# Kernel optimization log

Measured on AMD Instinct MI355X. Metric: run time of the kernel, lower is better.

## Reference

```python
import jax, jax.numpy as jnp
import numpy as np

EPS = 1e-6


def setup_inputs() -> dict:
    key = jax.random.key(0)
    k_x, k_qkv, k_proj = jax.random.split(key, 3)
    B, C, H, W, D = 4, 256, 16, 16, 16
    x = jax.random.normal(k_x, (B, C, H, W, D), dtype=jnp.float32)
    # 1x1 Conv3d == per-position linear; init roughly like torch conv default
    fan_in = C
    bound = 1.0 / np.sqrt(fan_in)
    qkv_w = jax.random.uniform(k_qkv, (3 * C, C), jnp.float32, -bound, bound)
    qkv_b = jnp.zeros((3 * C,), jnp.float32)
    proj_w = jax.random.uniform(k_proj, (C, C), jnp.float32, -bound, bound)
    proj_b = jnp.zeros((C,), jnp.float32)
    norm_gamma = jnp.ones((C,), jnp.float32)
    norm_beta = jnp.zeros((C,), jnp.float32)
    return {"x": x, "norm_gamma": norm_gamma, "norm_beta": norm_beta,
            "qkv_w": qkv_w, "qkv_b": qkv_b, "proj_w": proj_w, "proj_b": proj_b}


def reference(x, norm_gamma, norm_beta, qkv_w, qkv_b, proj_w, proj_b):
    B, C, H, W, D = x.shape
    N = H * W * D
    scale = float(C) ** -0.5

    # GroupNorm with num_groups=1: normalize over (C,H,W,D) per sample (biased var)
    mean = jnp.mean(x, axis=(1, 2, 3, 4), keepdims=True)
    var = jnp.mean(jnp.square(x - mean), axis=(1, 2, 3, 4), keepdims=True)
    xn = (x - mean) * jax.lax.rsqrt(var + EPS)
    xn = xn * norm_gamma[None, :, None, None, None] + norm_beta[None, :, None, None, None]

    xn_flat = xn.reshape(B, C, N)  # b c n
    # 1x1 conv == channel-mixing GEMM
    qkv = jnp.einsum('oc,bcn->bon', qkv_w, xn_flat) + qkv_b[None, :, None]  # [B, 3C, N]
    q, k, v = jnp.split(qkv, 3, axis=1)  # each [B, C, N]

    w = jnp.einsum('bcq,bck->bqk', q, k) * scale  # [B, N, N]
    w = jax.nn.softmax(w, axis=-1)
    h = jnp.einsum('bqk,bck->bcq', w, v)  # [B, C, N]

    h = jnp.einsum('oc,bcn->bon', proj_w, h) + proj_b[None, :, None]
    return x + h.reshape(B, C, H, W, D)
```

## Files before the change

### kernel.cpp

```cpp
#include <hip/hip_runtime.h>

typedef __attribute__((ext_vector_type(8))) short short8;
typedef __attribute__((ext_vector_type(4))) float f32x4;
typedef __attribute__((ext_vector_type(16))) float f32x16;
typedef __attribute__((ext_vector_type(4))) int i32x4;

__device__ __forceinline__ unsigned short f2bf(float f){
  union { float f; unsigned int u; } cv; cv.f = f;
  unsigned int u = cv.u;
  u = (u + 0x7fffu + ((u >> 16) & 1u)) >> 16;
  return (unsigned short)u;
}
__device__ __forceinline__ float bf2f(unsigned short h){
  union { unsigned int u; float f; } cv; cv.u = ((unsigned int)h) << 16;
  return cv.f;
}

typedef unsigned int u32g __attribute__((address_space(1)));
typedef unsigned int u32l __attribute__((address_space(3)));
__device__ __forceinline__ void gload16(const void* g, void* l){
  __builtin_amdgcn_global_load_lds((const u32g*)g, (u32l*)l, 16, 0, 0);
}

__device__ __forceinline__ unsigned int cvtpk_bf16(float lo, float hi){
  unsigned int r;
  asm("v_cvt_pk_bf16_f32 %0, %1, %2" : "=v"(r) : "v"(lo), "v"(hi));
  return r;
}
__device__ __forceinline__ unsigned int cvt2_fp8(float a, float b){
  unsigned int r;
  asm("v_cvt_pk_fp8_f32 %0, %1, %2" : "=v"(r) : "v"(a), "v"(b));
  return r;
}

#define BARRIER() asm volatile("s_barrier" ::: "memory")
#define WAITV(N)  asm volatile("s_waitcnt vmcnt(" #N ")" ::: "memory")
#define WAITLGKM0() asm volatile("s_waitcnt lgkmcnt(0)" ::: "memory")

__global__ __launch_bounds__(256) void fused_pre_k(const float* __restrict__ x,
                                                   float2* __restrict__ partial,
                                                   const float* __restrict__ qkv_w,
                                                   const float* __restrict__ qkv_b,
                                                   const float* __restrict__ proj_w,
                                                   unsigned short* __restrict__ Wqk,
                                                   unsigned short* __restrict__ Wv,
                                                   unsigned short* __restrict__ Wp,
                                                   float* __restrict__ bias_qk){
  const int blk = blockIdx.x;
  if (blk < 256){
    const int b = blk >> 6, xb = blk & 63;
    const float4* xp = (const float4*)(x + (size_t)b*1048576 + (size_t)xb*16384);
    float s = 0.f, sq = 0.f;
    #pragma unroll
    for (int i = 0; i < 16; ++i){
      float4 v = xp[threadIdx.x + i*256];
      s  += v.x + v.y + v.z + v.w;
      sq += v.x*v.x + v.y*v.y + v.z*v.z + v.w*v.w;
    }
    #pragma unroll
    for (int m = 1; m < 64; m <<= 1){ s += __shfl_xor(s, m); sq += __shfl_xor(sq, m); }
    __shared__ float2 acc[4];
    if ((threadIdx.x & 63) == 0) acc[threadIdx.x >> 6] = make_float2(s, sq);
    __syncthreads();
    if (threadIdx.x == 0){
      float S = 0.f, Q = 0.f;
      for (int i = 0; i < 4; ++i){ S += acc[i].x; Q += acc[i].y; }
      partial[b*64 + xb] = make_float2(S, Q);
    }
  } else {
    int id = (blk - 256) * 256 + threadIdx.x;
    if (id < 131072){
      Wqk[id] = f2bf(qkv_w[id]);
      if (id < 512) bias_qk[id] = qkv_b[id];
    } else if (id < 196608){
      Wv[id - 131072] = f2bf(qkv_w[id]);
    } else {
      int j = id - 196608;
      Wp[j] = f2bf(proj_w[j]);
    }
  }
}

__global__ __launch_bounds__(256) void norm_transpose_k(const float* __restrict__ x,
                                                        const float* __restrict__ gamma,
                                                        const float* __restrict__ beta,
                                                        const float2* __restrict__ partial,
                                                        unsigned short* __restrict__ xnt){
  __shared__ float tile[64][65];
  __shared__ float2 stt;
  const int b = blockIdx.z, n0 = blockIdx.x*64, c0 = blockIdx.y*64;
  const int t = threadIdx.x;
  if (t < 64){
    float2 p = partial[b*64 + t];
    float s = p.x, q = p.y;
    #pragma unroll
    for (int m = 1; m < 64; m <<= 1){ s += __shfl_xor(s, m); q += __shfl_xor(q, m); }
    if (t == 0){
      const float inv = 1.0f/1048576.0f;
      float mean = s*inv;
      float var  = q*inv - mean*mean;
      stt = make_float2(mean, rsqrtf(var + 1e-6f));
    }
  }
  __syncthreads();
  const float2 st = stt;
  const int col = t & 63, rb = t >> 6;
  #pragma unroll
  for (int i = 0; i < 16; ++i){
    int rr = i*4 + rb;
    float xv = x[((size_t)b*256 + c0 + rr)*4096 + n0 + col];
    tile[rr][col] = (xv - st.x) * st.y * gamma[c0+rr] + beta[c0+rr];
  }
  __syncthreads();
  #pragma unroll
  for (int i = 0; i < 16; ++i){
    int nr = i*4 + rb;
    xnt[((size_t)b*4096 + n0 + nr)*256 + c0 + col] = f2bf(tile[col][nr]);
  }
}

__global__ __launch_bounds__(256) void gemm_nt_k(const unsigned short* __restrict__ A,
                                                 const unsigned short* __restrict__ B,
                                                 int lda, int ldb, long sA, long sB,
                                                 const float* __restrict__ bias_m,
                                                 const float* __restrict__ bias_n,
                                                 const float* __restrict__ resid, long sR,
                                                 float* __restrict__ outF,
                                                 unsigned short* __restrict__ outB,
                                                 unsigned char* __restrict__ out8,
                                                 int ldc, long sC, int vtile){
  __shared__ unsigned short As[64][40];
  __shared__ unsigned short Bs[64][40];
  const int b  = blockIdx.z;
  const int m0 = blockIdx.x * 64, n0 = blockIdx.y * 64;
  const unsigned short* Ab = A + (size_t)b * sA;
  const unsigned short* Bb = B + (size_t)b * sB;
  const int t = threadIdx.x;
  const int lane = t & 63, w = t >> 6;
  const int g = lane >> 4, r = lane & 15;
  const int wm = (w >> 1) * 32, wn = (w & 1) * 32;
  const int lrow = t >> 2, lcol = (t & 3) * 8;
  f32x4 acc00 = {0,0,0,0}, acc01 = {0,0,0,0}, acc10 = {0,0,0,0}, acc11 = {0,0,0,0};
  for (int ks = 0; ks < 8; ++ks){
    short8 av = *(const short8*)(Ab + (size_t)(m0 + lrow) * lda + ks*32 + lcol);
    short8 bv = *(const short8*)(Bb + (size_t)(n0 + lrow) * ldb + ks*32 + lcol);
    __syncthreads();
    *(short8*)&As[lrow][lcol] = av;
    *(short8*)&Bs[lrow][lcol] = bv;
    __syncthreads();
    short8 af0 = *(const short8*)&As[wm + r][g*8];
    short8 af1 = *(const short8*)&As[wm + 16 + r][g*8];
    short8 bf0 = *(const short8*)&Bs[wn + r][g*8];
    short8 bf1 = *(const short8*)&Bs[wn + 16 + r][g*8];
    acc00 = __builtin_amdgcn_mfma_f32_16x16x32_bf16(af0, bf0, acc00, 0, 0, 0);
    acc01 = __builtin_amdgcn_mfma_f32_16x16x32_bf16(af0, bf1, acc01, 0, 0, 0);
    acc10 = __builtin_amdgcn_mfma_f32_16x16x32_bf16(af1, bf0, acc10, 0, 0, 0);
    acc11 = __builtin_amdgcn_mfma_f32_16x16x32_bf16(af1, bf1, acc11, 0, 0, 0);
  }
  f32x4 accs[2][2] = {{acc00, acc01},{acc10, acc11}};
  #pragma unroll
  for (int mi = 0; mi < 2; ++mi)
    #pragma unroll
    for (int ni = 0; ni < 2; ++ni)
      #pragma unroll
      for (int j = 0; j < 4; ++j){
        int gm = m0 + wm + mi*16 + g*4 + j;
        int gn = n0 + wn + ni*16 + r;
        float vv = accs[mi][ni][j];
        if (bias_m) vv += bias_m[gm];
        if (bias_n) vv += bias_n[gn];
        if (resid)  vv += resid[(size_t)b*sR + (size_t)gm*ldc + gn];
        if (out8){
          out8[(size_t)b*sC + (size_t)gm*ldc + gn] = (unsigned char)(cvt2_fp8(vv, vv) & 0xff);
        } else if (outB){
          size_t off;
          if (vtile)
            off = (size_t)b*sC + (size_t)(gn >> 4)*4096 + (size_t)(gm >> 5)*512
                + ((gn >> 3) & 1)*256 + (gm & 31)*8 + (gn & 7);
          else
            off = (size_t)b*sC + (size_t)gm*ldc + gn;
          outB[off] = f2bf(vv);
        } else {
          outF[(size_t)b*sC + (size_t)gm*ldc + gn] = vv;
        }
      }
}

__global__ __launch_bounds__(512, 1) void attn_k(const unsigned char* __restrict__ qk8,
                                                 const unsigned short* __restrict__ vt,
                                                 unsigned short* __restrict__ po,
                                                 float* __restrict__ ml){
  __shared__ __align__(16) char smem[114688];
  const int id = blockIdx.x;
  const int combo = id & 7, qb = id >> 3;
  const int b = combo >> 1, ks = combo & 1;
  const int q0 = qb * 128;
  const int t = threadIdx.x, lane = t & 63, w = t >> 6;
  const int qw = w >> 1, cg = w & 1;
  const int hi = lane >> 5, l31 = lane & 31;
  const unsigned char* qkb = qk8 + (size_t)b * 4096 * 512;
  const unsigned short* vtb = vt + (size_t)b * 1048576;
  char* Pb = smem + 98304;
  const float SQL2 = 0.0625f * 1.44269504088896340736f;

  unsigned long long qf[16];
  {
    const unsigned char* qrow = qkb + (size_t)(q0 + qw*32 + l31) * 512;
    #pragma unroll
    for (int s = 0; s < 16; ++s) qf[s] = *(const unsigned long long*)(qrow + s*16 + hi*8);
  }

  auto stageK = [&](int kt, char* buf){
    const int kbase = ks*2048 + kt*64;
    #pragma unroll
    for (int i2 = 0; i2 < 2; ++i2){
      int ci = w*128 + i2*64 + lane;
      int r = ci >> 4;
      const unsigned char* src = qkb + (size_t)(kbase + r)*512 + 256
                               + (((ci & 15) ^ (r & 15)) * 16);
      gload16(src, buf + w*2048 + i2*1024);
    }
  };
  auto stageV = [&](int kt, char* buf){
    const int kbase = ks*2048 + kt*64;
    #pragma unroll
    for (int i = 0; i < 4; ++i){
      int tix = w*4 + i;
      const unsigned short* src = vtb + (size_t)((kbase >> 4) + (tix >> 3))*4096
                                + (tix & 7)*512 + lane*8;
      gload16(src, buf + 16384 + tix*1024);
    }
  };
  stageK(0, smem);
  stageV(0, smem);

  f32x16 O[4];
  #pragma unroll
  for (int cb = 0; cb < 4; ++cb)
    #pragma unroll
    for (int jj = 0; jj < 16; ++jj) O[cb][jj] = 0.f;
  float lrun = 0.f;
  const int ksw = (l31 & 15) << 4;

  for (int kt = 0; kt < 32; ++kt){
    char* cur = smem + (kt & 1)*49152;
    char* nxt = smem + ((kt + 1) & 1)*49152;

    WAITV(4);
    BARRIER();

    f32x16 Sa, Sb;
    #pragma unroll
    for (int jj = 0; jj < 16; ++jj){ Sa[jj] = 0.f; Sb[jj] = 0.f; }
    const char* kp = cur + (cg*32 + l31)*256;
    __builtin_amdgcn_s_setprio(1);
    #pragma unroll
    for (int s = 0; s < 8; ++s){
      unsigned long long k0 = *(const unsigned long long*)(kp + (((2*s  )*16 + hi*8) ^ ksw));
      unsigned long long k1 = *(const unsigned long long*)(kp + (((2*s+1)*16 + hi*8) ^ ksw));
      Sa = __builtin_amdgcn_mfma_f32_32x32x16_fp8_fp8((long long)k0, (long long)qf[2*s  ], Sa, 0, 0, 0);
      Sb = __builtin_amdgcn_mfma_f32_32x32x16_fp8_fp8((long long)k1, (long long)qf[2*s+1], Sb, 0, 0, 0);
    }
    __builtin_amdgcn_s_setprio(0);

    int ktn = (kt < 31) ? kt + 1 : 31;
    stageK(ktn, nxt);

    float p[16];
    #pragma unroll
    for (int jj = 0; jj < 16; ++jj)
      p[jj] = __builtin_amdgcn_exp2f(fmaf(Sa[jj] + Sb[jj], SQL2, -24.0f));
    lrun += ((p[0]+p[1]) + (p[2]+p[3])) + ((p[4]+p[5]) + (p[6]+p[7]))
          + ((p[8]+p[9]) + (p[10]+p[11])) + ((p[12]+p[13]) + (p[14]+p[15]));
    unsigned int a0 = cvtpk_bf16(p[0],p[1]),   a1 = cvtpk_bf16(p[2],p[3]);
    unsigned int a2 = cvtpk_bf16(p[4],p[5]),   a3 = cvtpk_bf16(p[6],p[7]);
    unsigned int a4 = cvtpk_bf16(p[8],p[9]),   a5 = cvtpk_bf16(p[10],p[11]);
    unsigned int a6 = cvtpk_bf16(p[12],p[13]), a7 = cvtpk_bf16(p[14],p[15]);
    asm("v_permlane32_swap_b32 %0, %1" : "+v"(a0), "+v"(a2));
    asm("v_permlane32_swap_b32 %0, %1" : "+v"(a1), "+v"(a3));
    asm("v_permlane32_swap_b32 %0, %1" : "+v"(a4), "+v"(a6));
    asm("v_permlane32_swap_b32 %0, %1" : "+v"(a5), "+v"(a7));
    i32x4 u0 = {(int)a0,(int)a1,(int)a2,(int)a3};
    i32x4 u1 = {(int)a4,(int)a5,(int)a6,(int)a7};
    short8 pa0 = __builtin_bit_cast(short8, u0);
    short8 pa1 = __builtin_bit_cast(short8, u1);
    *(short8*)(Pb + (qw*4 + cg*2    )*1024 + lane*16) = pa0;
    *(short8*)(Pb + (qw*4 + cg*2 + 1)*1024 + lane*16) = pa1;

    WAITV(2);
    WAITLGKM0();
    BARRIER();

    stageV(ktn, nxt);

    short8 qb0 = *(const short8*)(Pb + (qw*4 + (1-cg)*2    )*1024 + lane*16);
    short8 qb1 = *(const short8*)(Pb + (qw*4 + (1-cg)*2 + 1)*1024 + lane*16);
    short8 pf0 = cg ? qb0 : pa0;
    short8 pf1 = cg ? qb1 : pa1;
    short8 pf2 = cg ? pa0 : qb0;
    short8 pf3 = cg ? pa1 : qb1;
    const char* Vt = cur + 16384;
    __builtin_amdgcn_s_setprio(1);
    #pragma unroll
    for (int cb = 0; cb < 4; ++cb){
      short8 v0 = *(const short8*)(Vt + (0*8 + cg*4 + cb)*1024 + lane*16);
      O[cb] = __builtin_amdgcn_mfma_f32_32x32x16_bf16(v0, pf0, O[cb], 0, 0, 0);
      short8 v1 = *(const short8*)(Vt + (1*8 + cg*4 + cb)*1024 + lane*16);
      O[cb] = __builtin_amdgcn_mfma_f32_32x32x16_bf16(v1, pf1, O[cb], 0, 0, 0);
      short8 v2 = *(const short8*)(Vt + (2*8 + cg*4 + cb)*1024 + lane*16);
      O[cb] = __builtin_amdgcn_mfma_f32_32x32x16_bf16(v2, pf2, O[cb], 0, 0, 0);
      short8 v3 = *(const short8*)(Vt + (3*8 + cg*4 + cb)*1024 + lane*16);
      O[cb] = __builtin_amdgcn_mfma_f32_32x32x16_bf16(v3, pf3, O[cb], 0, 0, 0);
    }
    __builtin_amdgcn_s_setprio(0);
  }
  WAITV(0);

  float lf = lrun + __shfl_xor(lrun, 32);
  const int qg = q0 + qw*32 + l31;
  unsigned short* pob = po + (size_t)combo * 1048576;
  #pragma unroll
  for (int cb = 0; cb < 4; ++cb)
    #pragma unroll
    for (int jj = 0; jj < 16; ++jj){
      int c = cg*128 + cb*32 + (jj & 3) + 8*(jj >> 2) + 4*hi;
      pob[(size_t)c*4096 + qg] = f2bf(O[cb][jj]);
    }
  if (lane < 32)
    ml[(size_t)(combo*2 + cg)*4096 + qg] = lf;
}

__global__ __launch_bounds__(256) void attn_merge_k(const unsigned short* __restrict__ po,
                                                    const float* __restrict__ ml,
                                                    unsigned short* __restrict__ ho){
  __shared__ float Of[64][261];
  const int b = blockIdx.y, q0 = blockIdx.x * 64;
  const int t = threadIdx.x, ql = t & 63, ci = t >> 6;
  const int q = q0 + ql;
  float L = ml[(size_t)((b*2+0)*2 + 0)*4096 + q] + ml[(size_t)((b*2+0)*2 + 1)*4096 + q]
          + ml[(size_t)((b*2+1)*2 + 0)*4096 + q] + ml[(size_t)((b*2+1)*2 + 1)*4096 + q];
  float inv = 1.0f / L;
  const unsigned short* p0 = po + (size_t)(b*2+0)*1048576 + q;
  const unsigned short* p1 = po + (size_t)(b*2+1)*1048576 + q;
  #pragma unroll
  for (int i = 0; i < 64; ++i){
    int c = ci + 4*i;
    float v = bf2f(p0[(size_t)c*4096]) + bf2f(p1[(size_t)c*4096]);
    Of[ql][c] = v * inv;
  }
  __syncthreads();
  const int qr = t >> 2, sub = t & 3;
  const float* rowp = Of[qr];
  unsigned short* dst = ho + ((size_t)(b*4096 + q0 + qr))*256;
  #pragma unroll
  for (int jj = 0; jj < 8; ++jj){
    int c = sub*8 + jj*32;
    float4 v0 = *(const float4*)(rowp + c);
    float4 v1 = *(const float4*)(rowp + c + 4);
    short8 o;
    o[0] = (short)f2bf(v0.x); o[1] = (short)f2bf(v0.y);
    o[2] = (short)f2bf(v0.z); o[3] = (short)f2bf(v0.w);
    o[4] = (short)f2bf(v1.x); o[5] = (short)f2bf(v1.y);
    o[6] = (short)f2bf(v1.z); o[7] = (short)f2bf(v1.w);
    *(short8*)(dst + c) = o;
  }
}

extern "C" void kernel_launch(void* const* d_in, const int* in_sizes, int n_in,
                              void* d_out, int out_size, void* d_ws, size_t ws_size,
                              hipStream_t stream){
  const float* x      = (const float*)d_in[0];
  const float* gamma  = (const float*)d_in[1];
  const float* beta   = (const float*)d_in[2];
  const float* qkv_w  = (const float*)d_in[3];
  const float* qkv_b  = (const float*)d_in[4];
  const float* proj_w = (const float*)d_in[5];
  const float* proj_b = (const float*)d_in[6];
  float* out = (float*)d_out;
  char* ws = (char*)d_ws;

  float2* partial        = (float2*)(ws + 0);
  float*  bias_qk        = (float*)(ws + 4096);
  unsigned short* Wqk    = (unsigned short*)(ws + 8192);
  unsigned short* Wv     = (unsigned short*)(ws + 270336);
  unsigned short* Wp     = (unsigned short*)(ws + 401408);
  unsigned short* xnt    = (unsigned short*)(ws + 532480);
  unsigned char*  qk8    = (unsigned char*)(ws + 8921088);
  unsigned short* vt     = (unsigned short*)(ws + 17309696);
  unsigned short* po     = (unsigned short*)(ws + 25698304);
  float*          ml     = (float*)(ws + 42475520);
  unsigned short* ho     = xnt;

  fused_pre_k<<<1280, 256, 0, stream>>>(x, partial, qkv_w, qkv_b, proj_w,
                                        Wqk, Wv, Wp, bias_qk);
  norm_transpose_k<<<dim3(64,4,4), 256, 0, stream>>>(x, gamma, beta, partial, xnt);
  gemm_nt_k<<<dim3(64,8,4), 256, 0, stream>>>(xnt, Wqk, 256, 256, 4096L*256, 0,
      nullptr, bias_qk, nullptr, 0, nullptr, nullptr, qk8, 512, 4096L*512, 0);
  gemm_nt_k<<<dim3(4,64,4), 256, 0, stream>>>(Wv, xnt, 256, 256, 0, 4096L*256,
      qkv_b + 512, nullptr, nullptr, 0, nullptr, vt, nullptr, 4096, 256L*4096, 1);
  attn_k<<<dim3(256), 512, 0, stream>>>(qk8, vt, po, ml);
  attn_merge_k<<<dim3(64,4), 256, 0, stream>>>(po, ml, ho);
  gemm_nt_k<<<dim3(4,64,4), 256, 0, stream>>>(Wp, ho, 256, 256, 0, 4096L*256,
      proj_b, nullptr, x, 1048576L, out, nullptr, nullptr, 4096, 1048576L, 0);
}
```

Before: 135.3 us.

## Split attention keys four ways with 32-key tiles and per-wave full channel output

The attention kernel now splits keys into four chunks instead of two, launching 512 blocks of 256 threads with two blocks per CU. Each wave holds all 256 output channels for its 32 queries, which removes the shared-memory exchange of P between wave pairs and the second barrier. Key tiles shrink to 32 and the next tile is prefetched right after a full wait, so the old split staging goes away. The cost is twice the O accumulators per wave (more register pressure), a fully drained wait each iteration, and a merge kernel that reads four partial outputs instead of two.

```diff
diff --git a/kernel.cpp b/kernel.cpp
--- a/kernel.cpp
+++ b/kernel.cpp
@@ -186,73 +186,75 @@
       }
 }
 
-__global__ __launch_bounds__(512, 1) void attn_k(const unsigned char* __restrict__ qk8,
+__global__ __launch_bounds__(256, 2) void attn_k(const unsigned char* __restrict__ qk8,
                                                  const unsigned short* __restrict__ vt,
                                                  unsigned short* __restrict__ po,
                                                  float* __restrict__ ml){
-  __shared__ __align__(16) char smem[114688];
+  __shared__ __align__(16) char smem[49152];
   const int id = blockIdx.x;
-  const int combo = id & 7, qb = id >> 3;
-  const int b = combo >> 1, ks = combo & 1;
+  const int combo = id & 15, qb = id >> 4;
+  const int b = combo >> 2, ks = combo & 3;
   const int q0 = qb * 128;
   const int t = threadIdx.x, lane = t & 63, w = t >> 6;
-  const int qw = w >> 1, cg = w & 1;
   const int hi = lane >> 5, l31 = lane & 31;
   const unsigned char* qkb = qk8 + (size_t)b * 4096 * 512;
   const unsigned short* vtb = vt + (size_t)b * 1048576;
-  char* Pb = smem + 98304;
   const float SQL2 = 0.0625f * 1.44269504088896340736f;
 
   unsigned long long qf[16];
   {
-    const unsigned char* qrow = qkb + (size_t)(q0 + qw*32 + l31) * 512;
+    const unsigned char* qrow = qkb + (size_t)(q0 + w*32 + l31) * 512;
     #pragma unroll
     for (int s = 0; s < 16; ++s) qf[s] = *(const unsigned long long*)(qrow + s*16 + hi*8);
   }
 
   auto stageK = [&](int kt, char* buf){
-    const int kbase = ks*2048 + kt*64;
+    const int kbase = ks*1024 + kt*32;
     #pragma unroll
     for (int i2 = 0; i2 < 2; ++i2){
-      int ci = w*128 + i2*64 + lane;
+      int ci = (w*2 + i2)*64 + lane;
       int r = ci >> 4;
       const unsigned char* src = qkb + (size_t)(kbase + r)*512 + 256
                                + (((ci & 15) ^ (r & 15)) * 16);
-      gload16(src, buf + w*2048 + i2*1024);
+      gload16(src, buf + (w*2 + i2)*1024);
     }
   };
   auto stageV = [&](int kt, char* buf){
-    const int kbase = ks*2048 + kt*64;
+    const int kbase = ks*1024 + kt*32;
     #pragma unroll
     for (int i = 0; i < 4; ++i){
       int tix = w*4 + i;
       const unsigned short* src = vtb + (size_t)((kbase >> 4) + (tix >> 3))*4096
                                 + (tix & 7)*512 + lane*8;
-      gload16(src, buf + 16384 + tix*1024);
+      gload16(src, buf + 8192 + tix*1024);
     }
   };
   stageK(0, smem);
   stageV(0, smem);
 
-  f32x16 O[4];
-  #pragma unroll
-  for (int cb = 0; cb < 4; ++cb)
+  f32x16 O[8];
+  #pragma unroll
+  for (int cb = 0; cb < 8; ++cb)
     #pragma unroll
     for (int jj = 0; jj < 16; ++jj) O[cb][jj] = 0.f;
   float lrun = 0.f;
   const int ksw = (l31 & 15) << 4;
 
   for (int kt = 0; kt < 32; ++kt){
-    char* cur = smem + (kt & 1)*49152;
-    char* nxt = smem + ((kt + 1) & 1)*49152;
-
-    WAITV(4);
+    char* cur = smem + (kt & 1)*24576;
+    char* nxt = smem + ((kt + 1) & 1)*24576;
+
+    WAITV(0);
     BARRIER();
 
+    int ktn = (kt < 31) ? kt + 1 : 31;
+    stageK(ktn, nxt);
+    stageV(ktn, nxt);
+
     f32x16 Sa, Sb;
     #pragma unroll
     for (int jj = 0; jj < 16; ++jj){ Sa[jj] = 0.f; Sb[jj] = 0.f; }
-    const char* kp = cur + (cg*32 + l31)*256;
+    const char* kp = cur + l31*256;
     __builtin_amdgcn_s_setprio(1);
     #pragma unroll
     for (int s = 0; s < 8; ++s){
@@ -262,9 +264,6 @@
       Sb = __builtin_amdgcn_mfma_f32_32x32x16_fp8_fp8((long long)k1, (long long)qf[2*s+1], Sb, 0, 0, 0);
     }
     __builtin_amdgcn_s_setprio(0);
-
-    int ktn = (kt < 31) ? kt + 1 : 31;
-    stageK(ktn, nxt);
 
     float p[16];
     #pragma unroll
@@ -284,50 +283,32 @@
     i32x4 u1 = {(int)a4,(int)a5,(int)a6,(int)a7};
     short8 pa0 = __builtin_bit_cast(short8, u0);
     short8 pa1 = __builtin_bit_cast(short8, u1);
-    *(short8*)(Pb + (qw*4 + cg*2    )*1024 + lane*16) = pa0;
-    *(short8*)(Pb + (qw*4 + cg*2 + 1)*1024 + lane*16) = pa1;
-
-    WAITV(2);
-    WAITLGKM0();
-    BARRIER();
-
-    stageV(ktn, nxt);
-
-    short8 qb0 = *(const short8*)(Pb + (qw*4 + (1-cg)*2    )*1024 + lane*16);
-    short8 qb1 = *(const short8*)(Pb + (qw*4 + (1-cg)*2 + 1)*1024 + lane*16);
-    short8 pf0 = cg ? qb0 : pa0;
-    short8 pf1 = cg ? qb1 : pa1;
-    short8 pf2 = cg ? pa0 : qb0;
-    short8 pf3 = cg ? pa1 : qb1;
-    const char* Vt = cur + 16384;
+
+    const char* Vt = cur + 8192;
     __builtin_amdgcn_s_setprio(1);
     #pragma unroll
-    for (int cb = 0; cb < 4; ++cb){
-      short8 v0 = *(const short8*)(Vt + (0*8 + cg*4 + cb)*1024 + lane*16);
-      O[cb] = __builtin_amdgcn_mfma_f32_32x32x16_bf16(v0, pf0, O[cb], 0, 0, 0);
-      short8 v1 = *(const short8*)(Vt + (1*8 + cg*4 + cb)*1024 + lane*16);
-      O[cb] = __builtin_amdgcn_mfma_f32_32x32x16_bf16(v1, pf1, O[cb], 0, 0, 0);
-      short8 v2 = *(const short8*)(Vt + (2*8 + cg*4 + cb)*1024 + lane*16);
-      O[cb] = __builtin_amdgcn_mfma_f32_32x32x16_bf16(v2, pf2, O[cb], 0, 0, 0);
-      short8 v3 = *(const short8*)(Vt + (3*8 + cg*4 + cb)*1024 + lane*16);
-      O[cb] = __builtin_amdgcn_mfma_f32_32x32x16_bf16(v3, pf3, O[cb], 0, 0, 0);
+    for (int cb = 0; cb < 8; ++cb){
+      short8 v0 = *(const short8*)(Vt + (0*8 + cb)*1024 + lane*16);
+      O[cb] = __builtin_amdgcn_mfma_f32_32x32x16_bf16(v0, pa0, O[cb], 0, 0, 0);
+      short8 v1 = *(const short8*)(Vt + (1*8 + cb)*1024 + lane*16);
+      O[cb] = __builtin_amdgcn_mfma_f32_32x32x16_bf16(v1, pa1, O[cb], 0, 0, 0);
     }
     __builtin_amdgcn_s_setprio(0);
   }
   WAITV(0);
 
   float lf = lrun + __shfl_xor(lrun, 32);
-  const int qg = q0 + qw*32 + l31;
+  const int qg = q0 + w*32 + l31;
   unsigned short* pob = po + (size_t)combo * 1048576;
   #pragma unroll
-  for (int cb = 0; cb < 4; ++cb)
+  for (int cb = 0; cb < 8; ++cb)
     #pragma unroll
     for (int jj = 0; jj < 16; ++jj){
-      int c = cg*128 + cb*32 + (jj & 3) + 8*(jj >> 2) + 4*hi;
+      int c = cb*32 + (jj & 3) + 8*(jj >> 2) + 4*hi;
       pob[(size_t)c*4096 + qg] = f2bf(O[cb][jj]);
     }
   if (lane < 32)
-    ml[(size_t)(combo*2 + cg)*4096 + qg] = lf;
+    ml[(size_t)combo*4096 + qg] = lf;
 }
 
 __global__ __launch_bounds__(256) void attn_merge_k(const unsigned short* __restrict__ po,
@@ -337,17 +318,23 @@
   const int b = blockIdx.y, q0 = blockIdx.x * 64;
   const int t = threadIdx.x, ql = t & 63, ci = t >> 6;
   const int q = q0 + ql;
-  float L = ml[(size_t)((b*2+0)*2 + 0)*4096 + q] + ml[(size_t)((b*2+0)*2 + 1)*4096 + q]
-          + ml[(size_t)((b*2+1)*2 + 0)*4096 + q] + ml[(size_t)((b*2+1)*2 + 1)*4096 + q];
+  float L = 0.f;
+  #pragma unroll
+  for (int ksv = 0; ksv < 4; ++ksv)
+    L += ml[(size_t)(b*4 + ksv)*4096 + q];
   float inv = 1.0f / L;
-  const unsigned short* p0 = po + (size_t)(b*2+0)*1048576 + q;
-  const unsigned short* p1 = po + (size_t)(b*2+1)*1048576 + q;
-  #pragma unroll
-  for (int i = 0; i < 64; ++i){
-    int c = ci + 4*i;
-    float v = bf2f(p0[(size_t)c*4096]) + bf2f(p1[(size_t)c*4096]);
-    Of[ql][c] = v * inv;
-  }
+  float acc[64];
+  #pragma unroll
+  for (int i = 0; i < 64; ++i) acc[i] = 0.f;
+  #pragma unroll
+  for (int ksv = 0; ksv < 4; ++ksv){
+    const unsigned short* pb = po + (size_t)(b*4 + ksv)*1048576 + q;
+    #pragma unroll
+    for (int i = 0; i < 64; ++i)
+      acc[i] += bf2f(pb[(size_t)(ci + 4*i)*4096]);
+  }
+  #pragma unroll
+  for (int i = 0; i < 64; ++i) Of[ql][ci + 4*i] = acc[i] * inv;
   __syncthreads();
   const int qr = t >> 2, sub = t & 3;
   const float* rowp = Of[qr];
@@ -388,7 +375,7 @@
   unsigned char*  qk8    = (unsigned char*)(ws + 8921088);
   unsigned short* vt     = (unsigned short*)(ws + 17309696);
   unsigned short* po     = (unsigned short*)(ws + 25698304);
-  float*          ml     = (float*)(ws + 42475520);
+  float*          ml     = (float*)(ws + 59252736);
   unsigned short* ho     = xnt;
 
   fused_pre_k<<<1280, 256, 0, stream>>>(x, partial, qkv_w, qkv_b, proj_w,
@@ -398,7 +385,7 @@
       nullptr, bias_qk, nullptr, 0, nullptr, nullptr, qk8, 512, 4096L*512, 0);
   gemm_nt_k<<<dim3(4,64,4), 256, 0, stream>>>(Wv, xnt, 256, 256, 0, 4096L*256,
       qkv_b + 512, nullptr, nullptr, 0, nullptr, vt, nullptr, 4096, 256L*4096, 1);
-  attn_k<<<dim3(256), 512, 0, stream>>>(qk8, vt, po, ml);
+  attn_k<<<dim3(512), 256, 0, stream>>>(qk8, vt, po, ml);
   attn_merge_k<<<dim3(64,4), 256, 0, stream>>>(po, ml, ho);
   gemm_nt_k<<<dim3(4,64,4), 256, 0, stream>>>(Wp, ho, 256, 256, 0, 4096L*256,
       proj_b, nullptr, x, 1048576L, out, nullptr, nullptr, 4096, 1048576L, 0);
```

Result: slower. 138.1 us (+2.1%).
